# Kernel tuning notes

Hardware: AMD Instinct MI355X
Metric: run time of the kernel (lower is better)

The kernel has to match this reference:

```python
import jax, jax.numpy as jnp
import numpy as np

B, S, D, H, L = 8, 2048, 512, 8, 5
DK = D // H
SP = S - L + 1  # number of local windows


def setup_inputs() -> dict:
    key = jax.random.key(0)
    ks = jax.random.split(key, 5)
    scale = 1.0 / np.sqrt(D).astype(np.float32)
    return {
        "query": jax.random.normal(ks[0], (B, S, D), dtype=jnp.float32),
        "key": jax.random.normal(ks[1], (B, S, D), dtype=jnp.float32),
        "value": jax.random.normal(ks[2], (B, S, D), dtype=jnp.float32),
        "W0": jax.random.normal(ks[3], (D, D), dtype=jnp.float32) * scale,
        "b0": jnp.zeros((D,), dtype=jnp.float32),
        "Wout": jax.random.normal(ks[4], (D, D), dtype=jnp.float32) * scale,
        "bout": jnp.zeros((D,), dtype=jnp.float32),
    }


def _local_agg(x, weighted):
    # x: (B, S, D). Sliding-window aggregation over windows of length L.
    # scores[b, t, s] = <x[b, t+L-1], x[b, s]> / sqrt(D)  -- per the source:
    # matmul(x[:, L-1:], x^T) / sqrt(d_model)
    scores = jnp.einsum("btd,bsd->bts", x[:, L - 1:], x) / (float(D) ** 0.5)
    idx = jnp.arange(SP)[:, None] + jnp.arange(L)[None, :]  # (SP, L)
    # per-window softmax over the L local scores
    w = jax.nn.softmax(jnp.take_along_axis(scores, idx[None, :, :], axis=-1), axis=-1)  # (B, SP, L)
    win = x[:, idx]  # (B, SP, L, D) gathered windows
    if weighted:
        win = w[..., None] * win
    return jnp.sum(win, axis=2)  # (B, SP, D)


def reference(query, key, value, W0, b0, Wout, bout):
    # Bug-faithful: the source overwrites the weighted query with the raw
    # windows (`query = q_list`), so query windows are summed UNweighted;
    # key windows use the local softmax weights.
    q = _local_agg(query, weighted=False)  # (B, SP, D)
    k = _local_agg(key, weighted=True)     # (B, SP, D)
    v = value[:, L - 1:] @ W0 + b0         # linears[0], aligned to SP positions

    def heads(t):  # (B, SP, D) -> (B, H, SP, DK)
        return t.reshape(t.shape[0], t.shape[1], H, DK).transpose(0, 2, 1, 3)

    qh, kh, vh = heads(q), heads(k), heads(v)
    att = jax.nn.softmax(jnp.einsum("bhtd,bhsd->bhts", qh, kh) / (float(DK) ** 0.5), axis=-1)
    x = jnp.einsum("bhts,bhsd->bhtd", att, vh)  # (B, H, SP, DK)
    x = x.transpose(0, 2, 1, 3).reshape(q.shape[0], SP, D)
    return x @ Wout + bout  # linears[-1]
```

## Files before the change

kernel.cpp:

```cpp
#include <hip/hip_runtime.h>
#include <hip/hip_bf16.h>
#include <hip/hip_fp16.h>

#define B_ 8
#define S_ 2048
#define D_ 512
#define H_ 8
#define L_ 5
#define DK_ 64
#define SP_ 2044
#define SPAD_ 2048

typedef _Float16 f16_t;
typedef _Float16 f16x4 __attribute__((ext_vector_type(4)));
typedef _Float16 f16x8 __attribute__((ext_vector_type(8)));
typedef __fp16 fp16x2_b __attribute__((ext_vector_type(2)));
typedef float f32x4 __attribute__((ext_vector_type(4)));
typedef float f32x16 __attribute__((ext_vector_type(16)));
typedef unsigned int u32;

static __device__ __forceinline__ f32x4 mfma16(f16x8 a, f16x8 b, f32x4 c) {
    return __builtin_amdgcn_mfma_f32_16x16x32_f16(a, b, c, 0, 0, 0);
}
static __device__ __forceinline__ f32x16 mfma32(f16x8 a, f16x8 b, f32x16 c) {
    return __builtin_amdgcn_mfma_f32_32x32x16_f16(a, b, c, 0, 0, 0);
}

union PK4 { f16x4 v; fp16x2_b h[2]; };
union U32H2 { u32 u; fp16x2_b h; };
union FRAG { uint4 u; f16x8 f; };

static __device__ __forceinline__ void swap32(u32 a, u32 b, u32& r0, u32& r1, int hi) {
#if __has_builtin(__builtin_amdgcn_permlane32_swap)
    auto r = __builtin_amdgcn_permlane32_swap(a, b, false, false);
    r0 = r[0]; r1 = r[1];
#else
    u32 t = __shfl_xor(hi ? a : b, 32, 64);
    r0 = hi ? t : a;
    r1 = hi ? b : t;
#endif
}

__global__ __launch_bounds__(256) void k_convert_w(
    const float* __restrict__ W0, const float* __restrict__ Wout,
    f16_t* __restrict__ WT0, f16_t* __restrict__ WT1) {
    int idx = blockIdx.x * 256 + threadIdx.x;
    int which = idx >> 18;
    int e = idx & 0x3FFFF;
    int k = e >> 9, n = e & 511;
    const float* W = which ? Wout : W0;
    f16_t* WT = which ? WT1 : WT0;
    WT[n * 512 + k] = (f16_t)W[k * 512 + n];
}

__global__ __launch_bounds__(256) void k_prep(
    const float* __restrict__ Qin, const float* __restrict__ Kin,
    f16_t* __restrict__ qh, f16_t* __restrict__ kh) {
    const int lane = threadIdx.x & 63;
    const int wid = threadIdx.x >> 6;
    const int gw = blockIdx.x * 4 + wid;
    const int b = gw >> 11;
    const int t = gw & 2047;
    const float* qb = Qin + (size_t)b * S_ * D_;
    const float* kb = Kin + (size_t)b * S_ * D_;
    const int d0 = lane * 8;

    float qs[8];
    float kl[5][8];
#pragma unroll
    for (int e = 0; e < 8; e++) qs[e] = 0.f;
#pragma unroll
    for (int l = 0; l < L_; l++) {
        int row = t + l; row = row < 2047 ? row : 2047;
        const float4* qp = (const float4*)(qb + (size_t)row * D_ + d0);
        float4 a = qp[0], c = qp[1];
        qs[0] += a.x; qs[1] += a.y; qs[2] += a.z; qs[3] += a.w;
        qs[4] += c.x; qs[5] += c.y; qs[6] += c.z; qs[7] += c.w;
        const float4* kp = (const float4*)(kb + (size_t)row * D_ + d0);
        float4 ka = kp[0], kc = kp[1];
        kl[l][0] = ka.x; kl[l][1] = ka.y; kl[l][2] = ka.z; kl[l][3] = ka.w;
        kl[l][4] = kc.x; kl[l][5] = kc.y; kl[l][6] = kc.z; kl[l][7] = kc.w;
    }
    float dot[5];
#pragma unroll
    for (int l = 0; l < 5; l++) {
        float d = 0.f;
#pragma unroll
        for (int e = 0; e < 8; e++) d += kl[4][e] * kl[l][e];
        dot[l] = d;
    }
#pragma unroll
    for (int m = 32; m; m >>= 1) {
#pragma unroll
        for (int l = 0; l < 5; l++) dot[l] += __shfl_xor(dot[l], m, 64);
    }
    const float sc = 0.044194173824159216f;
    float mx = dot[0];
#pragma unroll
    for (int l = 1; l < 5; l++) mx = fmaxf(mx, dot[l]);
    float w[5], sum = 0.f;
#pragma unroll
    for (int l = 0; l < 5; l++) { w[l] = __expf((dot[l] - mx) * sc); sum += w[l]; }
    float inv = 1.f / sum;
    float ks[8];
#pragma unroll
    for (int e = 0; e < 8; e++) {
        float v = 0.f;
#pragma unroll
        for (int l = 0; l < 5; l++) v += w[l] * kl[l][e];
        ks[e] = v * inv;
    }
    const int h = d0 >> 6, dk = d0 & 63;
    const size_t ob = ((size_t)(b * H_ + h) * SPAD_ + t) * DK_ + dk;
    const float qscale = 0.125f * 1.4426950408889634f;
    f16x8 qpk, kpk;
#pragma unroll
    for (int e = 0; e < 8; e++) {
        qpk[e] = (f16_t)(qs[e] * qscale);
        kpk[e] = (f16_t)ks[e];
    }
    *(f16x8*)(qh + ob) = qpk;
    *(f16x8*)(kh + ob) = kpk;
}

template <int MODE>
__global__ __launch_bounds__(256) void k_gemm(
    const void* __restrict__ Aptr, const f16_t* __restrict__ WT,
    const float* __restrict__ bias, void* __restrict__ Cptr) {
    __shared__ alignas(16) char smem[40960];
    const int tid = threadIdx.x, lane = tid & 63, wid = tid >> 6;
    const int mt = blockIdx.x >> 2, nt = blockIdx.x & 3;
    const int m0 = mt * 128, n0 = nt * 128;
    const int l15 = lane & 15, lg = lane >> 4;
    f32x4 acc[2][8] = {};

    const float* a0src = nullptr;
    const f16_t* a1src0 = nullptr, *a1src1 = nullptr;
    if (MODE == 0) {
        const float* A = (const float*)Aptr;
        int r = tid >> 1, cb = (tid & 1) * 16;
        int rp = m0 + r, b = rp >> 11, t = rp & 2047;
        int vrow = t + 4; vrow = vrow < 2047 ? vrow : 2047;
        a0src = A + ((size_t)b * 2048 + vrow) * 512 + cb;
    } else {
        const f16_t* A = (const f16_t*)Aptr;
        int r0 = tid >> 2, off0 = (tid & 3) * 8;
        int r1 = (tid + 256) >> 2;
        a1src0 = A + (size_t)(m0 + r0) * 512 + off0;
        a1src1 = A + (size_t)(m0 + r1) * 512 + off0;
    }
    const int bnl0 = tid >> 2, bko0 = (tid & 3) * 8;
    const int bnl1 = (tid + 256) >> 2;
    const f16_t* bsrc0 = WT + (size_t)(n0 + bnl0) * 512 + bko0;
    const f16_t* bsrc1 = WT + (size_t)(n0 + bnl1) * 512 + bko0;

    float4 fa[4];
    uint4 ua0, ua1, ub0, ub1;
    if (MODE == 0) {
#pragma unroll
        for (int j = 0; j < 4; j++) fa[j] = *(const float4*)(a0src + j * 4);
    } else {
        ua0 = *(const uint4*)a1src0;
        ua1 = *(const uint4*)a1src1;
    }
    ub0 = *(const uint4*)bsrc0;
    ub1 = *(const uint4*)bsrc1;

    for (int kt = 0; kt < 16; ++kt) {
        const int cur = kt & 1;
        f16_t (*Asm)[40] = (f16_t(*)[40])(smem + cur * 10240);
        f16_t (*Bsm)[40] = (f16_t(*)[40])(smem + 20480 + cur * 10240);
        if (MODE == 0) {
            int r = tid >> 1, cb = (tid & 1) * 16;
            f16x8 p0, p1;
            p0[0] = (f16_t)fa[0].x; p0[1] = (f16_t)fa[0].y; p0[2] = (f16_t)fa[0].z; p0[3] = (f16_t)fa[0].w;
            p0[4] = (f16_t)fa[1].x; p0[5] = (f16_t)fa[1].y; p0[6] = (f16_t)fa[1].z; p0[7] = (f16_t)fa[1].w;
            p1[0] = (f16_t)fa[2].x; p1[1] = (f16_t)fa[2].y; p1[2] = (f16_t)fa[2].z; p1[3] = (f16_t)fa[2].w;
            p1[4] = (f16_t)fa[3].x; p1[5] = (f16_t)fa[3].y; p1[6] = (f16_t)fa[3].z; p1[7] = (f16_t)fa[3].w;
            *(f16x8*)&Asm[r][cb] = p0;
            *(f16x8*)&Asm[r][cb + 8] = p1;
        } else {
            int r0 = tid >> 2, r1 = (tid + 256) >> 2, off = (tid & 3) * 8;
            *(uint4*)&Asm[r0][off] = ua0;
            *(uint4*)&Asm[r1][off] = ua1;
        }
        *(uint4*)&Bsm[bnl0][bko0] = ub0;
        *(uint4*)&Bsm[bnl1][bko0] = ub1;
        if (kt < 15) {
            const int k0n = (kt + 1) * 32;
            if (MODE == 0) {
#pragma unroll
                for (int j = 0; j < 4; j++) fa[j] = *(const float4*)(a0src + k0n + j * 4);
            } else {
                ua0 = *(const uint4*)(a1src0 + k0n);
                ua1 = *(const uint4*)(a1src1 + k0n);
            }
            ub0 = *(const uint4*)(bsrc0 + k0n);
            ub1 = *(const uint4*)(bsrc1 + k0n);
        }
        __syncthreads();
        f16x8 af[2], bfr[8];
#pragma unroll
        for (int i = 0; i < 2; i++) af[i] = *(const f16x8*)&Asm[wid * 32 + i * 16 + l15][lg * 8];
#pragma unroll
        for (int c = 0; c < 8; c++) bfr[c] = *(const f16x8*)&Bsm[c * 16 + l15][lg * 8];
        __builtin_amdgcn_s_setprio(1);
#pragma unroll
        for (int i = 0; i < 2; i++) {
#pragma unroll
            for (int c = 0; c < 8; c++) acc[i][c] = mfma16(af[i], bfr[c], acc[i][c]);
        }
        __builtin_amdgcn_s_setprio(0);
    }

    if (MODE == 0) {
        __syncthreads();
        f16_t (*Csm)[136] = (f16_t(*)[136])smem;
#pragma unroll
        for (int i = 0; i < 2; i++) {
#pragma unroll
            for (int c = 0; c < 8; c++) {
                int col = n0 + c * 16 + l15;
                float bv = bias[col];
                f16x4 pk;
#pragma unroll
                for (int r = 0; r < 4; r++) pk[r] = (f16_t)(acc[i][c][r] + bv);
                *(f16x4*)&Csm[c * 16 + l15][wid * 32 + i * 16 + lg * 4] = pk;
            }
        }
        __syncthreads();
        const int b = m0 >> 11, t0 = m0 & 2047;
        const int cl = tid >> 1, mo = (tid & 1) * 64;
        const int h = (n0 + cl) >> 6, dk = (n0 + cl) & 63;
        f16_t* dst = (f16_t*)Cptr + ((size_t)(b * H_ + h) * DK_ + dk) * SPAD_ + t0 + mo;
#pragma unroll
        for (int j = 0; j < 8; j++)
            *(uint4*)(dst + j * 8) = *(const uint4*)&Csm[cl][mo + j * 8];
    } else {
#pragma unroll
        for (int i = 0; i < 2; i++) {
#pragma unroll
            for (int c = 0; c < 8; c++) {
#pragma unroll
                for (int r = 0; r < 4; r++) {
                    int row = m0 + wid * 32 + i * 16 + lg * 4 + r;
                    int col = n0 + c * 16 + l15;
                    float v = acc[i][c][r] + bias[col];
                    int b = row >> 11, t = row & 2047;
                    if (t < SP_) {
                        float* outp = (float*)Cptr;
                        outp[((size_t)b * SP_ + t) * 512 + col] = v;
                    }
                }
            }
        }
    }
}

__global__ __launch_bounds__(256, 2) void k_attn(
    const f16_t* __restrict__ qh, const f16_t* __restrict__ kh,
    const f16_t* __restrict__ vhT, f16_t* __restrict__ xatt) {
    __shared__ alignas(16) f16_t Ksm[2][64][68];
    __shared__ alignas(16) f16_t Vsm[2][64][68];
    const int tid = threadIdx.x, lane = tid & 63, wid = tid >> 6;
    const int l31 = lane & 31, hi = lane >> 5, hi8 = hi * 8;
    const int vb = ((blockIdx.x & 7) << 6) | (blockIdx.x >> 3);
    const int bh = vb >> 3, qt = vb & 7;
    const f16_t* Q = qh + (size_t)bh * SPAD_ * DK_;
    const f16_t* K = kh + (size_t)bh * SPAD_ * DK_;
    const f16_t* VT = vhT + (size_t)bh * DK_ * SPAD_;
    const int qw = qt * 256 + wid * 64;

    f16x8 qf[2][4];
#pragma unroll
    for (int qg = 0; qg < 2; qg++)
#pragma unroll
        for (int kf = 0; kf < 4; kf++)
            qf[qg][kf] = *(const f16x8*)(Q + (size_t)(qw + qg * 32 + l31) * DK_ + kf * 16 + hi8);

    f32x16 cinit;
#pragma unroll
    for (int i = 0; i < 16; i++) cinit[i] = -12.f;

    f32x16 acc[2][2] = {};
    float rsa[2] = {0.f, 0.f}, rsb[2] = {0.f, 0.f};
    u32 pk[2][2][8];
    U32H2 one2; one2.u = 0x3C003C00u;

    const int sr = tid >> 3, so = (tid & 7) * 8;
    const f16_t* kg0 = K + (size_t)sr * DK_ + so;
    const f16_t* kg1 = K + (size_t)(sr + 32) * DK_ + so;
    const f16_t* vg0 = VT + (size_t)sr * SPAD_ + so;
    const f16_t* vg1 = VT + (size_t)(sr + 32) * SPAD_ + so;

    uint4 rk0 = *(const uint4*)kg0;
    uint4 rk1 = *(const uint4*)kg1;
    uint4 rv0 = *(const uint4*)vg0;
    uint4 rv1 = *(const uint4*)vg1;

    for (int t = 0; t < 32; ++t) {
        const int cur = t & 1;
        *(uint4*)&Ksm[cur][sr][so]      = rk0;
        *(uint4*)&Ksm[cur][sr + 32][so] = rk1;
        *(uint4*)&Vsm[cur][sr][so]      = rv0;
        *(uint4*)&Vsm[cur][sr + 32][so] = rv1;
        if (t < 31) {
            const int nxt = (t + 1) << 6;
            rk0 = *(const uint4*)(kg0 + (size_t)nxt * DK_);
            rk1 = *(const uint4*)(kg1 + (size_t)nxt * DK_);
            rv0 = *(const uint4*)(vg0 + nxt);
            rv1 = *(const uint4*)(vg1 + nxt);
        }
        __syncthreads();

#pragma unroll
        for (int kr = 0; kr < 2; ++kr) {
            f32x16 sv0 = cinit, sv1 = cinit;
            __builtin_amdgcn_s_setprio(1);
#pragma unroll
            for (int kf = 0; kf < 4; ++kf) {
                f16x8 a = *(const f16x8*)&Ksm[cur][kr * 32 + l31][kf * 16 + hi8];
                sv0 = mfma32(a, qf[0][kf], sv0);
                sv1 = mfma32(a, qf[1][kf], sv1);
            }
            __builtin_amdgcn_s_setprio(0);
            if (t == 31 && kr == 1) {
#pragma unroll
                for (int r = 12; r < 16; ++r) {
                    sv0[r] = hi ? -1e30f : sv0[r];
                    sv1[r] = hi ? -1e30f : sv1[r];
                }
            }
#pragma unroll
            for (int j = 0; j < 8; ++j) {
                float a0 = __builtin_amdgcn_exp2f(sv0[2 * j]);
                float a1 = __builtin_amdgcn_exp2f(sv0[2 * j + 1]);
                U32H2 c0; c0.h = __builtin_amdgcn_cvt_pkrtz(a0, a1);
                pk[0][kr][j] = c0.u;
                float b0 = __builtin_amdgcn_exp2f(sv1[2 * j]);
                float b1 = __builtin_amdgcn_exp2f(sv1[2 * j + 1]);
                U32H2 c1; c1.h = __builtin_amdgcn_cvt_pkrtz(b0, b1);
                pk[1][kr][j] = c1.u;
#if __has_builtin(__builtin_amdgcn_fdot2)
                if (j & 1) {
                    rsb[0] = __builtin_amdgcn_fdot2(c0.h, one2.h, rsb[0], false);
                    rsb[1] = __builtin_amdgcn_fdot2(c1.h, one2.h, rsb[1], false);
                } else {
                    rsa[0] = __builtin_amdgcn_fdot2(c0.h, one2.h, rsa[0], false);
                    rsa[1] = __builtin_amdgcn_fdot2(c1.h, one2.h, rsa[1], false);
                }
#else
                if (j & 1) { rsb[0] += a0 + a1; rsb[1] += b0 + b1; }
                else       { rsa[0] += a0 + a1; rsa[1] += b0 + b1; }
#endif
            }
        }

#pragma unroll
        for (int kc = 0; kc < 4; ++kc) {
            const int kr = kc >> 1, al = (kc & 1) * 4;
            FRAG p0, p1;
            {
                u32 m0, m1, m2, m3;
                swap32(pk[0][kr][al],     pk[0][kr][al + 2], m0, m2, hi);
                swap32(pk[0][kr][al + 1], pk[0][kr][al + 3], m1, m3, hi);
                p0.u = make_uint4(m0, m1, m2, m3);
                swap32(pk[1][kr][al],     pk[1][kr][al + 2], m0, m2, hi);
                swap32(pk[1][kr][al + 1], pk[1][kr][al + 3], m1, m3, hi);
                p1.u = make_uint4(m0, m1, m2, m3);
            }
            __builtin_amdgcn_s_setprio(1);
#pragma unroll
            for (int dc = 0; dc < 2; ++dc) {
                f16x8 v = *(const f16x8*)&Vsm[cur][dc * 32 + l31][kc * 16 + hi8];
                acc[0][dc] = mfma32(v, p0.f, acc[0][dc]);
                acc[1][dc] = mfma32(v, p1.f, acc[1][dc]);
            }
            __builtin_amdgcn_s_setprio(0);
        }
    }

    float rs0 = rsa[0] + rsb[0];
    float rs1 = rsa[1] + rsb[1];
    rs0 += __shfl_xor(rs0, 32, 64);
    rs1 += __shfl_xor(rs1, 32, 64);
    const float inv[2] = {1.f / rs0, 1.f / rs1};

    __syncthreads();
    f16_t (*Osm)[68] = (f16_t(*)[68])&Ksm[0][0][0];
#pragma unroll
    for (int qg = 0; qg < 2; ++qg) {
        const int row = wid * 64 + qg * 32 + l31;
#pragma unroll
        for (int dc = 0; dc < 2; ++dc) {
#pragma unroll
            for (int p = 0; p < 8; ++p) {
                float e0 = acc[qg][dc][2 * p] * inv[qg];
                float e1 = acc[qg][dc][2 * p + 1] * inv[qg];
                U32H2 c; c.h = __builtin_amdgcn_cvt_pkrtz(e0, e1);
                const int d = dc * 32 + 2 * (p & 1) + 8 * (p >> 1) + 4 * hi;
                *(u32*)&Osm[row][d] = c.u;
            }
        }
    }
    __syncthreads();
    const int b = bh >> 3, hh = bh & 7;
#pragma unroll
    for (int ps = 0; ps < 8; ++ps) {
        const int row = wid * 64 + ps * 8 + (lane >> 3);
        const int dco = (lane & 7) * 8;
        uint4 v = *(const uint4*)&Osm[row][dco];
        f16_t* dst = xatt + ((size_t)b * SPAD_ + qt * 256 + row) * D_ + hh * DK_ + dco;
        *(uint4*)dst = v;
    }
}

extern "C" void kernel_launch(void* const* d_in, const int* in_sizes, int n_in,
                              void* d_out, int out_size, void* d_ws, size_t ws_size,
                              hipStream_t stream) {
    const float* query = (const float*)d_in[0];
    const float* key   = (const float*)d_in[1];
    const float* value = (const float*)d_in[2];
    const float* W0    = (const float*)d_in[3];
    const float* b0    = (const float*)d_in[4];
    const float* Wout  = (const float*)d_in[5];
    const float* bout  = (const float*)d_in[6];
    float* out = (float*)d_out;

    char* w = (char*)d_ws;
    const size_t SZ = (size_t)B_ * H_ * SPAD_ * DK_ * sizeof(f16_t);
    f16_t* qh   = (f16_t*)w; w += SZ;
    f16_t* kh   = (f16_t*)w; w += SZ;
    f16_t* vhT  = (f16_t*)w; w += SZ;
    f16_t* xatt = (f16_t*)w; w += SZ;
    f16_t* WT0  = (f16_t*)w; w += (size_t)512 * 512 * sizeof(f16_t);
    f16_t* WT1  = (f16_t*)w; w += (size_t)512 * 512 * sizeof(f16_t);

    k_convert_w<<<2048, 256, 0, stream>>>(W0, Wout, WT0, WT1);
    k_prep<<<4096, 256, 0, stream>>>(query, key, qh, kh);
    k_gemm<0><<<512, 256, 0, stream>>>((const void*)value, WT0, b0, (void*)vhT);
    k_attn<<<512, 256, 0, stream>>>(qh, kh, vhT, xatt);
    k_gemm<1><<<512, 256, 0, stream>>>((const void*)xatt, WT1, bout, (void*)out);
}
```

Measured before the change: 154.2 us.

## Restructure GEMM and attention pipelines with single-barrier staging and halve attention query tile

The GEMM and attention main loops are reordered so the next tile is written to the alternate shared buffer after the MFMA work, and prefetched two steps ahead. A custom fence (lgkmcnt wait plus s_barrier with scheduling barriers) replaces __syncthreads, leaving one barrier per iteration. The attention kernel now gives each wave 32 query rows instead of 64, doubles the grid to 1024 blocks and raises launch bounds to 4 blocks per CU for occupancy. The cost is that K/V tiles are reloaded twice as often across blocks, and there is less MFMA work per wave to hide latency.

```diff
diff --git a/kernel.cpp b/kernel.cpp
--- a/kernel.cpp
+++ b/kernel.cpp
@@ -26,9 +26,16 @@
     return __builtin_amdgcn_mfma_f32_32x32x16_f16(a, b, c, 0, 0, 0);
 }
 
-union PK4 { f16x4 v; fp16x2_b h[2]; };
 union U32H2 { u32 u; fp16x2_b h; };
 union FRAG { uint4 u; f16x8 f; };
+
+#define PIPE_FENCE() do {                              \
+    __builtin_amdgcn_sched_barrier(0);                 \
+    asm volatile("s_waitcnt lgkmcnt(0)");              \
+    __builtin_amdgcn_sched_barrier(0);                 \
+    __builtin_amdgcn_s_barrier();                      \
+    __builtin_amdgcn_sched_barrier(0);                 \
+} while (0)
 
 static __device__ __forceinline__ void swap32(u32 a, u32 b, u32& r0, u32& r1, int hi) {
 #if __has_builtin(__builtin_amdgcn_permlane32_swap)
@@ -166,10 +173,9 @@
     ub0 = *(const uint4*)bsrc0;
     ub1 = *(const uint4*)bsrc1;
 
-    for (int kt = 0; kt < 16; ++kt) {
-        const int cur = kt & 1;
-        f16_t (*Asm)[40] = (f16_t(*)[40])(smem + cur * 10240);
-        f16_t (*Bsm)[40] = (f16_t(*)[40])(smem + 20480 + cur * 10240);
+    auto stage = [&](int buf) {
+        f16_t (*Asm)[40] = (f16_t(*)[40])(smem + buf * 10240);
+        f16_t (*Bsm)[40] = (f16_t(*)[40])(smem + 20480 + buf * 10240);
         if (MODE == 0) {
             int r = tid >> 1, cb = (tid & 1) * 16;
             f16x8 p0, p1;
@@ -186,19 +192,28 @@
         }
         *(uint4*)&Bsm[bnl0][bko0] = ub0;
         *(uint4*)&Bsm[bnl1][bko0] = ub1;
-        if (kt < 15) {
-            const int k0n = (kt + 1) * 32;
-            if (MODE == 0) {
-#pragma unroll
-                for (int j = 0; j < 4; j++) fa[j] = *(const float4*)(a0src + k0n + j * 4);
-            } else {
-                ua0 = *(const uint4*)(a1src0 + k0n);
-                ua1 = *(const uint4*)(a1src1 + k0n);
-            }
-            ub0 = *(const uint4*)(bsrc0 + k0n);
-            ub1 = *(const uint4*)(bsrc1 + k0n);
-        }
-        __syncthreads();
+    };
+    auto fetch = [&](int kt) {
+        const int k0n = kt * 32;
+        if (MODE == 0) {
+#pragma unroll
+            for (int j = 0; j < 4; j++) fa[j] = *(const float4*)(a0src + k0n + j * 4);
+        } else {
+            ua0 = *(const uint4*)(a1src0 + k0n);
+            ua1 = *(const uint4*)(a1src1 + k0n);
+        }
+        ub0 = *(const uint4*)(bsrc0 + k0n);
+        ub1 = *(const uint4*)(bsrc1 + k0n);
+    };
+
+    stage(0);
+    fetch(1);
+    PIPE_FENCE();
+
+    for (int kt = 0; kt < 16; ++kt) {
+        const int cur = kt & 1;
+        f16_t (*Asm)[40] = (f16_t(*)[40])(smem + cur * 10240);
+        f16_t (*Bsm)[40] = (f16_t(*)[40])(smem + 20480 + cur * 10240);
         f16x8 af[2], bfr[8];
 #pragma unroll
         for (int i = 0; i < 2; i++) af[i] = *(const f16x8*)&Asm[wid * 32 + i * 16 + l15][lg * 8];
@@ -211,6 +226,11 @@
             for (int c = 0; c < 8; c++) acc[i][c] = mfma16(af[i], bfr[c], acc[i][c]);
         }
         __builtin_amdgcn_s_setprio(0);
+        if (kt < 15) {
+            stage(cur ^ 1);
+            if (kt < 14) fetch(kt + 2);
+            PIPE_FENCE();
+        }
     }
 
     if (MODE == 0) {
@@ -257,34 +277,32 @@
     }
 }
 
-__global__ __launch_bounds__(256, 2) void k_attn(
+__global__ __launch_bounds__(256, 4) void k_attn(
     const f16_t* __restrict__ qh, const f16_t* __restrict__ kh,
     const f16_t* __restrict__ vhT, f16_t* __restrict__ xatt) {
     __shared__ alignas(16) f16_t Ksm[2][64][68];
     __shared__ alignas(16) f16_t Vsm[2][64][68];
     const int tid = threadIdx.x, lane = tid & 63, wid = tid >> 6;
     const int l31 = lane & 31, hi = lane >> 5, hi8 = hi * 8;
-    const int vb = ((blockIdx.x & 7) << 6) | (blockIdx.x >> 3);
-    const int bh = vb >> 3, qt = vb & 7;
+    const int vb = ((blockIdx.x & 7) << 7) | (blockIdx.x >> 3);
+    const int bh = vb >> 4, qt = vb & 15;
     const f16_t* Q = qh + (size_t)bh * SPAD_ * DK_;
     const f16_t* K = kh + (size_t)bh * SPAD_ * DK_;
     const f16_t* VT = vhT + (size_t)bh * DK_ * SPAD_;
-    const int qw = qt * 256 + wid * 64;
-
-    f16x8 qf[2][4];
-#pragma unroll
-    for (int qg = 0; qg < 2; qg++)
-#pragma unroll
-        for (int kf = 0; kf < 4; kf++)
-            qf[qg][kf] = *(const f16x8*)(Q + (size_t)(qw + qg * 32 + l31) * DK_ + kf * 16 + hi8);
+    const int qw = qt * 128 + wid * 32;
+
+    f16x8 qf[4];
+#pragma unroll
+    for (int kf = 0; kf < 4; kf++)
+        qf[kf] = *(const f16x8*)(Q + (size_t)(qw + l31) * DK_ + kf * 16 + hi8);
 
     f32x16 cinit;
 #pragma unroll
     for (int i = 0; i < 16; i++) cinit[i] = -12.f;
 
-    f32x16 acc[2][2] = {};
-    float rsa[2] = {0.f, 0.f}, rsb[2] = {0.f, 0.f};
-    u32 pk[2][2][8];
+    f32x16 acc[2] = {};
+    float rsa = 0.f, rsb = 0.f;
+    u32 pk[2][8];
     U32H2 one2; one2.u = 0x3C003C00u;
 
     const int sr = tid >> 3, so = (tid & 7) * 8;
@@ -297,61 +315,45 @@
     uint4 rk1 = *(const uint4*)kg1;
     uint4 rv0 = *(const uint4*)vg0;
     uint4 rv1 = *(const uint4*)vg1;
+    *(uint4*)&Ksm[0][sr][so]      = rk0;
+    *(uint4*)&Ksm[0][sr + 32][so] = rk1;
+    *(uint4*)&Vsm[0][sr][so]      = rv0;
+    *(uint4*)&Vsm[0][sr + 32][so] = rv1;
+    rk0 = *(const uint4*)(kg0 + (size_t)64 * DK_);
+    rk1 = *(const uint4*)(kg1 + (size_t)64 * DK_);
+    rv0 = *(const uint4*)(vg0 + 64);
+    rv1 = *(const uint4*)(vg1 + 64);
+    PIPE_FENCE();
 
     for (int t = 0; t < 32; ++t) {
         const int cur = t & 1;
-        *(uint4*)&Ksm[cur][sr][so]      = rk0;
-        *(uint4*)&Ksm[cur][sr + 32][so] = rk1;
-        *(uint4*)&Vsm[cur][sr][so]      = rv0;
-        *(uint4*)&Vsm[cur][sr + 32][so] = rv1;
-        if (t < 31) {
-            const int nxt = (t + 1) << 6;
-            rk0 = *(const uint4*)(kg0 + (size_t)nxt * DK_);
-            rk1 = *(const uint4*)(kg1 + (size_t)nxt * DK_);
-            rv0 = *(const uint4*)(vg0 + nxt);
-            rv1 = *(const uint4*)(vg1 + nxt);
-        }
-        __syncthreads();
 
 #pragma unroll
         for (int kr = 0; kr < 2; ++kr) {
-            f32x16 sv0 = cinit, sv1 = cinit;
+            f32x16 sv = cinit;
             __builtin_amdgcn_s_setprio(1);
 #pragma unroll
             for (int kf = 0; kf < 4; ++kf) {
                 f16x8 a = *(const f16x8*)&Ksm[cur][kr * 32 + l31][kf * 16 + hi8];
-                sv0 = mfma32(a, qf[0][kf], sv0);
-                sv1 = mfma32(a, qf[1][kf], sv1);
+                sv = mfma32(a, qf[kf], sv);
             }
             __builtin_amdgcn_s_setprio(0);
             if (t == 31 && kr == 1) {
 #pragma unroll
-                for (int r = 12; r < 16; ++r) {
-                    sv0[r] = hi ? -1e30f : sv0[r];
-                    sv1[r] = hi ? -1e30f : sv1[r];
-                }
+                for (int r = 12; r < 16; ++r) sv[r] = hi ? -1e30f : sv[r];
             }
 #pragma unroll
             for (int j = 0; j < 8; ++j) {
-                float a0 = __builtin_amdgcn_exp2f(sv0[2 * j]);
-                float a1 = __builtin_amdgcn_exp2f(sv0[2 * j + 1]);
+                float a0 = __builtin_amdgcn_exp2f(sv[2 * j]);
+                float a1 = __builtin_amdgcn_exp2f(sv[2 * j + 1]);
                 U32H2 c0; c0.h = __builtin_amdgcn_cvt_pkrtz(a0, a1);
-                pk[0][kr][j] = c0.u;
-                float b0 = __builtin_amdgcn_exp2f(sv1[2 * j]);
-                float b1 = __builtin_amdgcn_exp2f(sv1[2 * j + 1]);
-                U32H2 c1; c1.h = __builtin_amdgcn_cvt_pkrtz(b0, b1);
-                pk[1][kr][j] = c1.u;
+                pk[kr][j] = c0.u;
 #if __has_builtin(__builtin_amdgcn_fdot2)
-                if (j & 1) {
-                    rsb[0] = __builtin_amdgcn_fdot2(c0.h, one2.h, rsb[0], false);
-                    rsb[1] = __builtin_amdgcn_fdot2(c1.h, one2.h, rsb[1], false);
-                } else {
-                    rsa[0] = __builtin_amdgcn_fdot2(c0.h, one2.h, rsa[0], false);
-                    rsa[1] = __builtin_amdgcn_fdot2(c1.h, one2.h, rsa[1], false);
-                }
+                if (j & 1) rsb = __builtin_amdgcn_fdot2(c0.h, one2.h, rsb, false);
+                else       rsa = __builtin_amdgcn_fdot2(c0.h, one2.h, rsa, false);
 #else
-                if (j & 1) { rsb[0] += a0 + a1; rsb[1] += b0 + b1; }
-                else       { rsa[0] += a0 + a1; rsa[1] += b0 + b1; }
+                if (j & 1) rsb += a0 + a1;
+                else       rsa += a0 + a1;
 #endif
             }
         }
@@ -359,44 +361,53 @@
 #pragma unroll
         for (int kc = 0; kc < 4; ++kc) {
             const int kr = kc >> 1, al = (kc & 1) * 4;
-            FRAG p0, p1;
+            FRAG p;
             {
                 u32 m0, m1, m2, m3;
-                swap32(pk[0][kr][al],     pk[0][kr][al + 2], m0, m2, hi);
-                swap32(pk[0][kr][al + 1], pk[0][kr][al + 3], m1, m3, hi);
-                p0.u = make_uint4(m0, m1, m2, m3);
-                swap32(pk[1][kr][al],     pk[1][kr][al + 2], m0, m2, hi);
-                swap32(pk[1][kr][al + 1], pk[1][kr][al + 3], m1, m3, hi);
-                p1.u = make_uint4(m0, m1, m2, m3);
+                swap32(pk[kr][al],     pk[kr][al + 2], m0, m2, hi);
+                swap32(pk[kr][al + 1], pk[kr][al + 3], m1, m3, hi);
+                p.u = make_uint4(m0, m1, m2, m3);
             }
             __builtin_amdgcn_s_setprio(1);
 #pragma unroll
             for (int dc = 0; dc < 2; ++dc) {
                 f16x8 v = *(const f16x8*)&Vsm[cur][dc * 32 + l31][kc * 16 + hi8];
-                acc[0][dc] = mfma32(v, p0.f, acc[0][dc]);
-                acc[1][dc] = mfma32(v, p1.f, acc[1][dc]);
+                acc[dc] = mfma32(v, p.f, acc[dc]);
             }
             __builtin_amdgcn_s_setprio(0);
         }
-    }
-
-    float rs0 = rsa[0] + rsb[0];
-    float rs1 = rsa[1] + rsb[1];
-    rs0 += __shfl_xor(rs0, 32, 64);
-    rs1 += __shfl_xor(rs1, 32, 64);
-    const float inv[2] = {1.f / rs0, 1.f / rs1};
+
+        if (t < 31) {
+            const int nb = cur ^ 1;
+            *(uint4*)&Ksm[nb][sr][so]      = rk0;
+            *(uint4*)&Ksm[nb][sr + 32][so] = rk1;
+            *(uint4*)&Vsm[nb][sr][so]      = rv0;
+            *(uint4*)&Vsm[nb][sr + 32][so] = rv1;
+            if (t < 30) {
+                const int nxt = (t + 2) << 6;
+                rk0 = *(const uint4*)(kg0 + (size_t)nxt * DK_);
+                rk1 = *(const uint4*)(kg1 + (size_t)nxt * DK_);
+                rv0 = *(const uint4*)(vg0 + nxt);
+                rv1 = *(const uint4*)(vg1 + nxt);
+            }
+            PIPE_FENCE();
+        }
+    }
+
+    float rs = rsa + rsb;
+    rs += __shfl_xor(rs, 32, 64);
+    const float inv = 1.f / rs;
 
     __syncthreads();
     f16_t (*Osm)[68] = (f16_t(*)[68])&Ksm[0][0][0];
-#pragma unroll
-    for (int qg = 0; qg < 2; ++qg) {
-        const int row = wid * 64 + qg * 32 + l31;
+    {
+        const int row = wid * 32 + l31;
 #pragma unroll
         for (int dc = 0; dc < 2; ++dc) {
 #pragma unroll
             for (int p = 0; p < 8; ++p) {
-                float e0 = acc[qg][dc][2 * p] * inv[qg];
-                float e1 = acc[qg][dc][2 * p + 1] * inv[qg];
+                float e0 = acc[dc][2 * p] * inv;
+                float e1 = acc[dc][2 * p + 1] * inv;
                 U32H2 c; c.h = __builtin_amdgcn_cvt_pkrtz(e0, e1);
                 const int d = dc * 32 + 2 * (p & 1) + 8 * (p >> 1) + 4 * hi;
                 *(u32*)&Osm[row][d] = c.u;
@@ -406,11 +417,11 @@
     __syncthreads();
     const int b = bh >> 3, hh = bh & 7;
 #pragma unroll
-    for (int ps = 0; ps < 8; ++ps) {
-        const int row = wid * 64 + ps * 8 + (lane >> 3);
-        const int dco = (lane & 7) * 8;
+    for (int j = 0; j < 4; ++j) {
+        const int lin = tid + j * 256;
+        const int row = lin >> 3, dco = (lin & 7) * 8;
         uint4 v = *(const uint4*)&Osm[row][dco];
-        f16_t* dst = xatt + ((size_t)b * SPAD_ + qt * 256 + row) * D_ + hh * DK_ + dco;
+        f16_t* dst = xatt + ((size_t)b * SPAD_ + qt * 128 + row) * D_ + hh * DK_ + dco;
         *(uint4*)dst = v;
     }
 }
@@ -439,6 +450,6 @@
     k_convert_w<<<2048, 256, 0, stream>>>(W0, Wout, WT0, WT1);
     k_prep<<<4096, 256, 0, stream>>>(query, key, qh, kh);
     k_gemm<0><<<512, 256, 0, stream>>>((const void*)value, WT0, b0, (void*)vhT);
-    k_attn<<<512, 256, 0, stream>>>(qh, kh, vhT, xatt);
+    k_attn<<<1024, 256, 0, stream>>>(qh, kh, vhT, xatt);
     k_gemm<1><<<512, 256, 0, stream>>>((const void*)xatt, WT1, bout, (void*)out);
 }
```

After: 160.5 us. +4.1%, slower.

## Give each wave private K/V LDS buffers to drop block barriers in attention

Applied to the files above, without the earlier changes.

The attention kernel now has each wave fetch and stage its own 32-key K and V^T tiles into a private double-buffered LDS region. This removes the per-iteration __syncthreads, so the four waves no longer wait on each other. The loop runs 64 iterations over smaller tiles, with register prefetch two tiles ahead. The cost is that every wave loads the same K/V data, which quadruples global/L2 read traffic and LDS store work. Register usage may also rise because of the extra prefetch registers.

```diff
diff --git a/kernel.cpp b/kernel.cpp
--- a/kernel.cpp
+++ b/kernel.cpp
@@ -26,7 +26,6 @@
     return __builtin_amdgcn_mfma_f32_32x32x16_f16(a, b, c, 0, 0, 0);
 }
 
-union PK4 { f16x4 v; fp16x2_b h[2]; };
 union U32H2 { u32 u; fp16x2_b h; };
 union FRAG { uint4 u; f16x8 f; };
 
@@ -260,8 +259,8 @@
 __global__ __launch_bounds__(256, 2) void k_attn(
     const f16_t* __restrict__ qh, const f16_t* __restrict__ kh,
     const f16_t* __restrict__ vhT, f16_t* __restrict__ xatt) {
-    __shared__ alignas(16) f16_t Ksm[2][64][68];
-    __shared__ alignas(16) f16_t Vsm[2][64][68];
+    __shared__ alignas(16) f16_t Ksm[4][2][32][68];
+    __shared__ alignas(16) f16_t Vsm[4][2][64][36];
     const int tid = threadIdx.x, lane = tid & 63, wid = tid >> 6;
     const int l31 = lane & 31, hi = lane >> 5, hi8 = hi * 8;
     const int vb = ((blockIdx.x & 7) << 6) | (blockIdx.x >> 3);
@@ -271,136 +270,180 @@
     const f16_t* VT = vhT + (size_t)bh * DK_ * SPAD_;
     const int qw = qt * 256 + wid * 64;
 
-    f16x8 qf[2][4];
-#pragma unroll
-    for (int qg = 0; qg < 2; qg++)
-#pragma unroll
-        for (int kf = 0; kf < 4; kf++)
-            qf[qg][kf] = *(const f16x8*)(Q + (size_t)(qw + qg * 32 + l31) * DK_ + kf * 16 + hi8);
+    f16x8 qf00 = *(const f16x8*)(Q + (size_t)(qw + l31) * DK_ + 0  + hi8);
+    f16x8 qf01 = *(const f16x8*)(Q + (size_t)(qw + l31) * DK_ + 16 + hi8);
+    f16x8 qf02 = *(const f16x8*)(Q + (size_t)(qw + l31) * DK_ + 32 + hi8);
+    f16x8 qf03 = *(const f16x8*)(Q + (size_t)(qw + l31) * DK_ + 48 + hi8);
+    f16x8 qf10 = *(const f16x8*)(Q + (size_t)(qw + 32 + l31) * DK_ + 0  + hi8);
+    f16x8 qf11 = *(const f16x8*)(Q + (size_t)(qw + 32 + l31) * DK_ + 16 + hi8);
+    f16x8 qf12 = *(const f16x8*)(Q + (size_t)(qw + 32 + l31) * DK_ + 32 + hi8);
+    f16x8 qf13 = *(const f16x8*)(Q + (size_t)(qw + 32 + l31) * DK_ + 48 + hi8);
 
     f32x16 cinit;
 #pragma unroll
     for (int i = 0; i < 16; i++) cinit[i] = -12.f;
 
-    f32x16 acc[2][2] = {};
-    float rsa[2] = {0.f, 0.f}, rsb[2] = {0.f, 0.f};
-    u32 pk[2][2][8];
+    f32x16 accA0 = {}, accA1 = {};
+    f32x16 accB0 = {}, accB1 = {};
+    float rsa0 = 0.f, rsb0 = 0.f, rsa1 = 0.f, rsb1 = 0.f;
     U32H2 one2; one2.u = 0x3C003C00u;
 
-    const int sr = tid >> 3, so = (tid & 7) * 8;
-    const f16_t* kg0 = K + (size_t)sr * DK_ + so;
-    const f16_t* kg1 = K + (size_t)(sr + 32) * DK_ + so;
-    const f16_t* vg0 = VT + (size_t)sr * SPAD_ + so;
-    const f16_t* vg1 = VT + (size_t)(sr + 32) * SPAD_ + so;
-
-    uint4 rk0 = *(const uint4*)kg0;
-    uint4 rk1 = *(const uint4*)kg1;
-    uint4 rv0 = *(const uint4*)vg0;
-    uint4 rv1 = *(const uint4*)vg1;
-
-    for (int t = 0; t < 32; ++t) {
+    const int krow = l31, khalf = (lane >> 5) * 32;
+    const f16_t* kgb = K + (size_t)krow * DK_ + khalf;
+    const f16_t* vgb = VT + (size_t)lane * SPAD_;
+    uint4 rk0, rk1, rv0, rv1;
+
+    uint4 rk2, rk3, rv2, rv3;
+
+#define FETCH(T) do { const size_t ko_ = (size_t)(T) * 32 * DK_;          \
+    const int vo_ = (T) * 32;                                             \
+    rk0 = *(const uint4*)(kgb + ko_);                                     \
+    rk1 = *(const uint4*)(kgb + ko_ + 8);                                 \
+    rk2 = *(const uint4*)(kgb + ko_ + 16);                                \
+    rk3 = *(const uint4*)(kgb + ko_ + 24);                                \
+    rv0 = *(const uint4*)(vgb + vo_);                                     \
+    rv1 = *(const uint4*)(vgb + vo_ + 8);                                 \
+    rv2 = *(const uint4*)(vgb + vo_ + 16);                                \
+    rv3 = *(const uint4*)(vgb + vo_ + 24); } while (0)
+#define STAGE(BUF) do {                                                   \
+    *(uint4*)&Ksm[wid][BUF][krow][khalf]      = rk0;                      \
+    *(uint4*)&Ksm[wid][BUF][krow][khalf + 8]  = rk1;                      \
+    *(uint4*)&Ksm[wid][BUF][krow][khalf + 16] = rk2;                      \
+    *(uint4*)&Ksm[wid][BUF][krow][khalf + 24] = rk3;                      \
+    *(uint4*)&Vsm[wid][BUF][lane][0]  = rv0;                              \
+    *(uint4*)&Vsm[wid][BUF][lane][8]  = rv1;                              \
+    *(uint4*)&Vsm[wid][BUF][lane][16] = rv2;                              \
+    *(uint4*)&Vsm[wid][BUF][lane][24] = rv3; } while (0)
+
+#define QK(CUR, SV, Q0, Q1, Q2, Q3) do {                                  \
+    __builtin_amdgcn_s_setprio(1);                                        \
+    {                                                                     \
+        f16x8 a0_ = *(const f16x8*)&Ksm[wid][CUR][l31][0  + hi8];         \
+        SV = mfma32(a0_, Q0, cinit);                                      \
+        f16x8 a1_ = *(const f16x8*)&Ksm[wid][CUR][l31][16 + hi8];         \
+        SV = mfma32(a1_, Q1, SV);                                         \
+        f16x8 a2_ = *(const f16x8*)&Ksm[wid][CUR][l31][32 + hi8];         \
+        SV = mfma32(a2_, Q2, SV);                                         \
+        f16x8 a3_ = *(const f16x8*)&Ksm[wid][CUR][l31][48 + hi8];         \
+        SV = mfma32(a3_, Q3, SV);                                         \
+    }                                                                     \
+    __builtin_amdgcn_s_setprio(0);                                        \
+} while (0)
+
+#if __has_builtin(__builtin_amdgcn_fdot2)
+#define EXPPAIR(SV, J, T, RS) do {                                        \
+    float e0_ = __builtin_amdgcn_exp2f(SV[2 * (J)]);                      \
+    float e1_ = __builtin_amdgcn_exp2f(SV[2 * (J) + 1]);                  \
+    U32H2 c_; c_.h = __builtin_amdgcn_cvt_pkrtz(e0_, e1_);                \
+    T = c_.u;                                                             \
+    RS = __builtin_amdgcn_fdot2(c_.h, one2.h, RS, false);                 \
+} while (0)
+#else
+#define EXPPAIR(SV, J, T, RS) do {                                        \
+    float e0_ = __builtin_amdgcn_exp2f(SV[2 * (J)]);                      \
+    float e1_ = __builtin_amdgcn_exp2f(SV[2 * (J) + 1]);                  \
+    U32H2 c_; c_.h = __builtin_amdgcn_cvt_pkrtz(e0_, e1_);                \
+    T = c_.u;                                                             \
+    RS += e0_ + e1_;                                                      \
+} while (0)
+#endif
+
+#define EXP16(SV, PLO, PHI, RSA, RSB) do {                                \
+    u32 t0_, t1_, t2_, t3_, t4_, t5_, t6_, t7_;                           \
+    EXPPAIR(SV, 0, t0_, RSA); EXPPAIR(SV, 1, t1_, RSB);                   \
+    EXPPAIR(SV, 2, t2_, RSA); EXPPAIR(SV, 3, t3_, RSB);                   \
+    EXPPAIR(SV, 4, t4_, RSA); EXPPAIR(SV, 5, t5_, RSB);                   \
+    EXPPAIR(SV, 6, t6_, RSA); EXPPAIR(SV, 7, t7_, RSB);                   \
+    PLO = make_uint4(t0_, t1_, t2_, t3_);                                 \
+    PHI = make_uint4(t4_, t5_, t6_, t7_);                                 \
+} while (0)
+
+#define PV_KC(CUR, PKU, KC, ACC0, ACC1) do {                              \
+    u32 m0_, m1_, m2_, m3_;                                               \
+    swap32(PKU.x, PKU.z, m0_, m2_, hi);                                   \
+    swap32(PKU.y, PKU.w, m1_, m3_, hi);                                   \
+    FRAG p_; p_.u = make_uint4(m0_, m1_, m2_, m3_);                       \
+    __builtin_amdgcn_s_setprio(1);                                        \
+    {                                                                     \
+        f16x8 v0_ = *(const f16x8*)&Vsm[wid][CUR][l31][(KC) * 16 + hi8];  \
+        ACC0 = mfma32(v0_, p_.f, ACC0);                                   \
+        f16x8 v1_ = *(const f16x8*)&Vsm[wid][CUR][32 + l31][(KC) * 16 + hi8]; \
+        ACC1 = mfma32(v1_, p_.f, ACC1);                                   \
+    }                                                                     \
+    __builtin_amdgcn_s_setprio(0);                                        \
+} while (0)
+
+    FETCH(0);
+    STAGE(0);
+    FETCH(1);
+
+    for (int t = 0; t < 64; ++t) {
         const int cur = t & 1;
-        *(uint4*)&Ksm[cur][sr][so]      = rk0;
-        *(uint4*)&Ksm[cur][sr + 32][so] = rk1;
-        *(uint4*)&Vsm[cur][sr][so]      = rv0;
-        *(uint4*)&Vsm[cur][sr + 32][so] = rv1;
-        if (t < 31) {
-            const int nxt = (t + 1) << 6;
-            rk0 = *(const uint4*)(kg0 + (size_t)nxt * DK_);
-            rk1 = *(const uint4*)(kg1 + (size_t)nxt * DK_);
-            rv0 = *(const uint4*)(vg0 + nxt);
-            rv1 = *(const uint4*)(vg1 + nxt);
-        }
-        __syncthreads();
-
-#pragma unroll
-        for (int kr = 0; kr < 2; ++kr) {
-            f32x16 sv0 = cinit, sv1 = cinit;
-            __builtin_amdgcn_s_setprio(1);
-#pragma unroll
-            for (int kf = 0; kf < 4; ++kf) {
-                f16x8 a = *(const f16x8*)&Ksm[cur][kr * 32 + l31][kf * 16 + hi8];
-                sv0 = mfma32(a, qf[0][kf], sv0);
-                sv1 = mfma32(a, qf[1][kf], sv1);
+        if (t < 63) {
+            STAGE(cur ^ 1);
+            if (t < 62) FETCH(t + 2);
+        }
+        f32x16 sv0, sv1;
+        QK(cur, sv0, qf00, qf01, qf02, qf03);
+        QK(cur, sv1, qf10, qf11, qf12, qf13);
+        if (t == 63) {
+#pragma unroll
+            for (int r = 12; r < 16; ++r) {
+                sv0[r] = hi ? -1e30f : sv0[r];
+                sv1[r] = hi ? -1e30f : sv1[r];
             }
-            __builtin_amdgcn_s_setprio(0);
-            if (t == 31 && kr == 1) {
-#pragma unroll
-                for (int r = 12; r < 16; ++r) {
-                    sv0[r] = hi ? -1e30f : sv0[r];
-                    sv1[r] = hi ? -1e30f : sv1[r];
-                }
-            }
-#pragma unroll
-            for (int j = 0; j < 8; ++j) {
-                float a0 = __builtin_amdgcn_exp2f(sv0[2 * j]);
-                float a1 = __builtin_amdgcn_exp2f(sv0[2 * j + 1]);
-                U32H2 c0; c0.h = __builtin_amdgcn_cvt_pkrtz(a0, a1);
-                pk[0][kr][j] = c0.u;
-                float b0 = __builtin_amdgcn_exp2f(sv1[2 * j]);
-                float b1 = __builtin_amdgcn_exp2f(sv1[2 * j + 1]);
-                U32H2 c1; c1.h = __builtin_amdgcn_cvt_pkrtz(b0, b1);
-                pk[1][kr][j] = c1.u;
-#if __has_builtin(__builtin_amdgcn_fdot2)
-                if (j & 1) {
-                    rsb[0] = __builtin_amdgcn_fdot2(c0.h, one2.h, rsb[0], false);
-                    rsb[1] = __builtin_amdgcn_fdot2(c1.h, one2.h, rsb[1], false);
-                } else {
-                    rsa[0] = __builtin_amdgcn_fdot2(c0.h, one2.h, rsa[0], false);
-                    rsa[1] = __builtin_amdgcn_fdot2(c1.h, one2.h, rsa[1], false);
-                }
-#else
-                if (j & 1) { rsb[0] += a0 + a1; rsb[1] += b0 + b1; }
-                else       { rsa[0] += a0 + a1; rsa[1] += b0 + b1; }
-#endif
-            }
-        }
-
-#pragma unroll
-        for (int kc = 0; kc < 4; ++kc) {
-            const int kr = kc >> 1, al = (kc & 1) * 4;
-            FRAG p0, p1;
-            {
-                u32 m0, m1, m2, m3;
-                swap32(pk[0][kr][al],     pk[0][kr][al + 2], m0, m2, hi);
-                swap32(pk[0][kr][al + 1], pk[0][kr][al + 3], m1, m3, hi);
-                p0.u = make_uint4(m0, m1, m2, m3);
-                swap32(pk[1][kr][al],     pk[1][kr][al + 2], m0, m2, hi);
-                swap32(pk[1][kr][al + 1], pk[1][kr][al + 3], m1, m3, hi);
-                p1.u = make_uint4(m0, m1, m2, m3);
-            }
-            __builtin_amdgcn_s_setprio(1);
-#pragma unroll
-            for (int dc = 0; dc < 2; ++dc) {
-                f16x8 v = *(const f16x8*)&Vsm[cur][dc * 32 + l31][kc * 16 + hi8];
-                acc[0][dc] = mfma32(v, p0.f, acc[0][dc]);
-                acc[1][dc] = mfma32(v, p1.f, acc[1][dc]);
-            }
-            __builtin_amdgcn_s_setprio(0);
-        }
-    }
-
-    float rs0 = rsa[0] + rsb[0];
-    float rs1 = rsa[1] + rsb[1];
+        }
+        uint4 pL0, pH0, pL1, pH1;
+        EXP16(sv0, pL0, pH0, rsa0, rsb0);
+        EXP16(sv1, pL1, pH1, rsa1, rsb1);
+        PV_KC(cur, pL0, 0, accA0, accA1);
+        PV_KC(cur, pH0, 1, accA0, accA1);
+        PV_KC(cur, pL1, 0, accB0, accB1);
+        PV_KC(cur, pH1, 1, accB0, accB1);
+    }
+
+    float rs0 = rsa0 + rsb0;
+    float rs1 = rsa1 + rsb1;
     rs0 += __shfl_xor(rs0, 32, 64);
     rs1 += __shfl_xor(rs1, 32, 64);
-    const float inv[2] = {1.f / rs0, 1.f / rs1};
+    const float inv0 = 1.f / rs0, inv1 = 1.f / rs1;
 
     __syncthreads();
-    f16_t (*Osm)[68] = (f16_t(*)[68])&Ksm[0][0][0];
-#pragma unroll
-    for (int qg = 0; qg < 2; ++qg) {
-        const int row = wid * 64 + qg * 32 + l31;
-#pragma unroll
-        for (int dc = 0; dc < 2; ++dc) {
-#pragma unroll
-            for (int p = 0; p < 8; ++p) {
-                float e0 = acc[qg][dc][2 * p] * inv[qg];
-                float e1 = acc[qg][dc][2 * p + 1] * inv[qg];
-                U32H2 c; c.h = __builtin_amdgcn_cvt_pkrtz(e0, e1);
-                const int d = dc * 32 + 2 * (p & 1) + 8 * (p >> 1) + 4 * hi;
-                *(u32*)&Osm[row][d] = c.u;
-            }
+    f16_t (*Osm)[68] = (f16_t(*)[68])&Ksm[0][0][0][0];
+    {
+        const int row0 = wid * 64 + l31;
+#pragma unroll
+        for (int p = 0; p < 8; ++p) {
+            float e0 = accA0[2 * p] * inv0;
+            float e1 = accA0[2 * p + 1] * inv0;
+            U32H2 c; c.h = __builtin_amdgcn_cvt_pkrtz(e0, e1);
+            const int d = 2 * (p & 1) + 8 * (p >> 1) + 4 * hi;
+            *(u32*)&Osm[row0][d] = c.u;
+        }
+#pragma unroll
+        for (int p = 0; p < 8; ++p) {
+            float e0 = accA1[2 * p] * inv0;
+            float e1 = accA1[2 * p + 1] * inv0;
+            U32H2 c; c.h = __builtin_amdgcn_cvt_pkrtz(e0, e1);
+            const int d = 32 + 2 * (p & 1) + 8 * (p >> 1) + 4 * hi;
+            *(u32*)&Osm[row0][d] = c.u;
+        }
+        const int row1 = wid * 64 + 32 + l31;
+#pragma unroll
+        for (int p = 0; p < 8; ++p) {
+            float e0 = accB0[2 * p] * inv1;
+            float e1 = accB0[2 * p + 1] * inv1;
+            U32H2 c; c.h = __builtin_amdgcn_cvt_pkrtz(e0, e1);
+            const int d = 2 * (p & 1) + 8 * (p >> 1) + 4 * hi;
+            *(u32*)&Osm[row1][d] = c.u;
+        }
+#pragma unroll
+        for (int p = 0; p < 8; ++p) {
+            float e0 = accB1[2 * p] * inv1;
+            float e1 = accB1[2 * p + 1] * inv1;
+            U32H2 c; c.h = __builtin_amdgcn_cvt_pkrtz(e0, e1);
+            const int d = 32 + 2 * (p & 1) + 8 * (p >> 1) + 4 * hi;
+            *(u32*)&Osm[row1][d] = c.u;
         }
     }
     __syncthreads();
@@ -413,6 +456,12 @@
         f16_t* dst = xatt + ((size_t)b * SPAD_ + qt * 256 + row) * D_ + hh * DK_ + dco;
         *(uint4*)dst = v;
     }
+#undef FETCH
+#undef STAGE
+#undef QK
+#undef EXPPAIR
+#undef EXP16
+#undef PV_KC
 }
 
 extern "C" void kernel_launch(void* const* d_in, const int* in_sizes, int n_in,
```

Measured after the change: 201.6 us. 30.7% more time.
